# Performance work log

Measured on AMD Instinct MI355X. Metric: run time of the kernel, lower is better.

## Reference

```python
import jax, jax.numpy as jnp
import numpy as np

D_MODEL = 1024
N_HEADS = 16
HEAD_DIM = D_MODEL // N_HEADS


def setup_inputs() -> dict:
    key = jax.random.key(0)
    ks = jax.random.split(key, 5)
    x = jax.random.normal(ks[0], (2, 2048, D_MODEL), dtype=jnp.float32)
    s = 1.0 / np.sqrt(D_MODEL)
    W_qkv = jax.random.normal(ks[1], (D_MODEL, 3 * D_MODEL), dtype=jnp.float32) * s
    b_qkv = jnp.zeros((3 * D_MODEL,), dtype=jnp.float32)
    W_proj = jax.random.normal(ks[2], (D_MODEL, D_MODEL), dtype=jnp.float32) * s
    b_proj = jnp.zeros((D_MODEL,), dtype=jnp.float32)
    return {"x": x, "W_qkv": W_qkv, "b_qkv": b_qkv, "W_proj": W_proj, "b_proj": b_proj}


def reference(x, W_qkv, b_qkv, W_proj, b_proj):
    b, t, c = x.shape
    qkv = x @ W_qkv + b_qkv  # [b,t,3c]
    q, k, v = jnp.split(qkv, 3, axis=-1)
    # [b, h, t, d]
    q = q.reshape(b, t, N_HEADS, HEAD_DIM).transpose(0, 2, 1, 3)
    k = k.reshape(b, t, N_HEADS, HEAD_DIM).transpose(0, 2, 1, 3)
    v = v.reshape(b, t, N_HEADS, HEAD_DIM).transpose(0, 2, 1, 3)
    att = jnp.einsum('bhqd,bhkd->bhqk', q, k) / np.sqrt(HEAD_DIM)
    causal = jnp.tril(jnp.ones((t, t), dtype=bool))  # [t,t]
    att = jnp.where(causal[None, None], att, -jnp.inf)
    att = jax.nn.softmax(att, axis=-1)
    out = jnp.einsum('bhqk,bhkd->bhqd', att, v)  # [b,h,t,d]
    out = out.transpose(0, 2, 1, 3).reshape(b, t, c)
    return out @ W_proj + b_proj
```

## Files before the change

### kernel.cpp

```cpp
#include <hip/hip_runtime.h>
#include <hip/hip_bf16.h>

#define NB 2
#define NH 16
#define HD 64
#define DM 1024
#define TT 2048

typedef __attribute__((ext_vector_type(4))) float f32x4;
typedef __attribute__((ext_vector_type(8))) short bf16x8;

__device__ __forceinline__ unsigned short f2bf(float f) {
  union { float f; unsigned int i; } x; x.f = f;
  unsigned int r = x.i + 0x7fffu + ((x.i >> 16) & 1u);
  return (unsigned short)(r >> 16);
}

__device__ __forceinline__ unsigned int cvtpk(float lo, float hi) {
  unsigned int r;
  asm("v_cvt_pk_bf16_f32 %0, %1, %2" : "=v"(r) : "v"(lo), "v"(hi));
  return r;
}

__device__ __forceinline__ void async16(unsigned short* lds_base, const unsigned short* g) {
  __builtin_amdgcn_global_load_lds(
      (const __attribute__((address_space(1))) void*)g,
      (__attribute__((address_space(3))) void*)lds_base, 16, 0, 0);
}

__global__ __launch_bounds__(256)
void prep_kernel(const float* __restrict__ x, unsigned short* __restrict__ xbf,
                 const float* __restrict__ Wqkv, unsigned short* __restrict__ WqkvT,
                 const float* __restrict__ Wproj, unsigned short* __restrict__ WprojT)
{
  __shared__ unsigned short T[64][72];
  const int bid = blockIdx.x;
  const int t = threadIdx.x;

  if (bid < 2048) {
    const int i = bid * 256 + t;
    const f32x4 a = *(const f32x4*)(x + (size_t)i * 8);
    const f32x4 b = *(const f32x4*)(x + (size_t)i * 8 + 4);
    uint4 o;
    o.x = f2bf(a.x) | ((unsigned)f2bf(a.y) << 16);
    o.y = f2bf(a.z) | ((unsigned)f2bf(a.w) << 16);
    o.z = f2bf(b.x) | ((unsigned)f2bf(b.y) << 16);
    o.w = f2bf(b.z) | ((unsigned)f2bf(b.w) << 16);
    *(uint4*)(xbf + (size_t)i * 8) = o;
    return;
  }

  const float* W;
  unsigned short* WT;
  int n0, k0, N;
  if (bid < 2048 + 768) {
    const int li = bid - 2048;
    W = Wqkv; WT = WqkvT; N = 3 * DM;
    n0 = (li % 48) * 64; k0 = (li / 48) * 64;
  } else {
    const int li = bid - 2816;
    W = Wproj; WT = WprojT; N = DM;
    n0 = (li % 16) * 64; k0 = (li / 16) * 64;
  }
  const int r = t >> 2;
  const int c = (t & 3) * 16;
  const float* src = W + (size_t)(k0 + r) * N + n0 + c;
  #pragma unroll
  for (int s = 0; s < 4; ++s) {
    const f32x4 v = *(const f32x4*)(src + s * 4);
    T[c + s*4 + 0][r] = f2bf(v.x);
    T[c + s*4 + 1][r] = f2bf(v.y);
    T[c + s*4 + 2][r] = f2bf(v.z);
    T[c + s*4 + 3][r] = f2bf(v.w);
  }
  __syncthreads();
  unsigned short* dst = WT + (size_t)(n0 + r) * DM + k0 + c;
  *(uint4*)(dst)     = *(const uint4*)(&T[r][c]);
  *(uint4*)(dst + 8) = *(const uint4*)(&T[r][c + 8]);
}

template<int MODE>
__global__ __launch_bounds__(256)
void gemm_bf16(const unsigned short* __restrict__ A, const unsigned short* __restrict__ BT,
               const float* __restrict__ bias, void* __restrict__ Cout,
               int M, int N, int K)
{
  __shared__ unsigned short As[128 * 32];
  __shared__ unsigned short Bs[128 * 32];
  const int tid = threadIdx.x;
  const int lane = tid & 63;
  const int w = tid >> 6;
  const int wr = w >> 1, wc = w & 1;
  const int l15 = lane & 15, g = lane >> 4;

  const int gx = gridDim.x;
  const int li = blockIdx.y * gx + blockIdx.x;
  const int chunk = (gx * gridDim.y) >> 3;
  const int tile = (li & 7) * chunk + (li >> 3);
  const int m0 = (tile / gx) * 128;
  const int n0 = (tile % gx) * 128;

  f32x4 acc[4][4] = {};

  const int ar0 = tid >> 2,          as0 = (tid & 3) * 8;
  const int ar1 = (256 + tid) >> 2;
  const unsigned short* A0 = A + (size_t)(m0 + ar0) * K + as0;
  const unsigned short* A1 = A + (size_t)(m0 + ar1) * K + as0;
  const unsigned short* B0 = BT + (size_t)(n0 + ar0) * K + as0;
  const unsigned short* B1 = BT + (size_t)(n0 + ar1) * K + as0;
  unsigned short* AsW0 = &As[(0 * 256 + w * 64) * 8];
  unsigned short* AsW1 = &As[(1 * 256 + w * 64) * 8];
  unsigned short* BsW0 = &Bs[(0 * 256 + w * 64) * 8];
  unsigned short* BsW1 = &Bs[(1 * 256 + w * 64) * 8];

  for (int k0 = 0; k0 < K; k0 += 32) {
    async16(AsW0, A0 + k0);
    async16(AsW1, A1 + k0);
    async16(BsW0, B0 + k0);
    async16(BsW1, B1 + k0);
    __syncthreads();

    bf16x8 af[4], bfv[4];
    #pragma unroll
    for (int i = 0; i < 4; ++i)
      af[i] = *(const bf16x8*)(&As[(wr * 64 + i * 16 + l15) * 32 + g * 8]);
    #pragma unroll
    for (int j = 0; j < 4; ++j)
      bfv[j] = *(const bf16x8*)(&Bs[(wc * 64 + j * 16 + l15) * 32 + g * 8]);
    #pragma unroll
    for (int i = 0; i < 4; ++i)
      #pragma unroll
      for (int j = 0; j < 4; ++j)
        acc[i][j] = __builtin_amdgcn_mfma_f32_16x16x32_bf16(af[i], bfv[j], acc[i][j], 0, 0, 0);
    __syncthreads();
  }

  #pragma unroll
  for (int i = 0; i < 4; ++i) {
    #pragma unroll
    for (int j = 0; j < 4; ++j) {
      #pragma unroll
      for (int e = 0; e < 4; ++e) {
        const int row = m0 + wr * 64 + i * 16 + g * 4 + e;
        const int col = n0 + wc * 64 + j * 16 + l15;
        float val = acc[i][j][e] + bias[col];
        if (MODE == 0) {
          const int which = col >> 10;
          if (which == 0) val *= 0.125f;
          const int rem = col & 1023;
          const int hh = rem >> 6, dd = rem & 63;
          const int bb = row >> 11, tt = row & 2047;
          ((unsigned short*)Cout)[((((size_t)which * NB + bb) * NH + hh) * TT + tt) * HD + dd] = f2bf(val);
        } else {
          ((float*)Cout)[(size_t)row * N + col] = val;
        }
      }
    }
  }
}

__global__ __launch_bounds__(512)
void attn_kernel(const unsigned short* __restrict__ qkv, unsigned short* __restrict__ attn_out)
{
  __shared__ unsigned short Ksm[64 * 72];
  __shared__ unsigned short VTsm[64 * 70];
  __shared__ unsigned short Psm[8][16 * 72];

  const int tid = threadIdx.x;
  const int lane = tid & 63;
  const int wv = tid >> 6;
  const int l15 = lane & 15;
  const int g = lane >> 4;

  const int li = blockIdx.x;
  const int xcd = li & 7;
  const int r = li >> 3;
  const int halfid = r >> 5;
  const int j = r & 31;
  const int bh = ((j >> 3) << 3) | xcd;
  const int jj = j & 7;
  const int qt = halfid ? (7 - jj) : (8 + jj);
  const int q0 = qt * 128;

  const size_t base = (size_t)bh * TT * HD;
  const unsigned short* Qg = qkv + base;
  const unsigned short* Kg = qkv + (size_t)NB * NH * TT * HD + base;
  const unsigned short* Vg = qkv + (size_t)2 * NB * NH * TT * HD + base;

  const int qw = q0 + wv * 16;
  const bf16x8 qf0 = *(const bf16x8*)(Qg + (size_t)(qw + l15) * HD + g * 8);
  const bf16x8 qf1 = *(const bf16x8*)(Qg + (size_t)(qw + l15) * HD + 32 + g * 8);

  f32x4 o[4] = {};
  float lsum = 0.f;

  const bool kRole = (wv < 4);
  const int krow = (tid & 255) >> 2;
  const int kseg = (tid & 3) * 16;
  const int vt   = tid & 255;
  const int vr0  = (vt >> 4) * 4;
  const int vc0  = (vt & 15) * 4;

  const int nt = 2 * qt + 2;

  uint4 st0, st1;
  {
    if (kRole) {
      const unsigned short* kp = Kg + (size_t)krow * HD + kseg;
      st0 = *(const uint4*)(kp);
      st1 = *(const uint4*)(kp + 8);
    } else {
      const uint2 a = *(const uint2*)(Vg + (size_t)(vr0 + 0) * HD + vc0);
      const uint2 b = *(const uint2*)(Vg + (size_t)(vr0 + 1) * HD + vc0);
      const uint2 c = *(const uint2*)(Vg + (size_t)(vr0 + 2) * HD + vc0);
      const uint2 d = *(const uint2*)(Vg + (size_t)(vr0 + 3) * HD + vc0);
      st0.x = a.x; st0.y = a.y; st0.z = b.x; st0.w = b.y;
      st1.x = c.x; st1.y = c.y; st1.z = d.x; st1.w = d.y;
    }
  }

  for (int t = 0; t < nt; ++t) {
    const int t0 = t * 64;
    __syncthreads();
    if (kRole) {
      *(uint4*)(&Ksm[krow * 72 + kseg])     = st0;
      *(uint4*)(&Ksm[krow * 72 + kseg + 8]) = st1;
    } else {
      unsigned short r0[4] = {(unsigned short)(st0.x & 0xffffu), (unsigned short)(st0.x >> 16),
                              (unsigned short)(st0.y & 0xffffu), (unsigned short)(st0.y >> 16)};
      unsigned short r1[4] = {(unsigned short)(st0.z & 0xffffu), (unsigned short)(st0.z >> 16),
                              (unsigned short)(st0.w & 0xffffu), (unsigned short)(st0.w >> 16)};
      unsigned short r2[4] = {(unsigned short)(st1.x & 0xffffu), (unsigned short)(st1.x >> 16),
                              (unsigned short)(st1.y & 0xffffu), (unsigned short)(st1.y >> 16)};
      unsigned short r3[4] = {(unsigned short)(st1.z & 0xffffu), (unsigned short)(st1.z >> 16),
                              (unsigned short)(st1.w & 0xffffu), (unsigned short)(st1.w >> 16)};
      #pragma unroll
      for (int c2 = 0; c2 < 4; ++c2) {
        ushort4 col;
        col.x = r0[c2]; col.y = r1[c2]; col.z = r2[c2]; col.w = r3[c2];
        *(ushort4*)(&VTsm[(vc0 + c2) * 70 + vr0]) = col;
      }
    }
    __syncthreads();

    if (t + 1 < nt) {
      const int t1 = t0 + 64;
      if (kRole) {
        const unsigned short* kp = Kg + (size_t)(t1 + krow) * HD + kseg;
        st0 = *(const uint4*)(kp);
        st1 = *(const uint4*)(kp + 8);
      } else {
        const uint2 a = *(const uint2*)(Vg + (size_t)(t1 + vr0 + 0) * HD + vc0);
        const uint2 b = *(const uint2*)(Vg + (size_t)(t1 + vr0 + 1) * HD + vc0);
        const uint2 c = *(const uint2*)(Vg + (size_t)(t1 + vr0 + 2) * HD + vc0);
        const uint2 d = *(const uint2*)(Vg + (size_t)(t1 + vr0 + 3) * HD + vc0);
        st0.x = a.x; st0.y = a.y; st0.z = b.x; st0.w = b.y;
        st1.x = c.x; st1.y = c.y; st1.z = d.x; st1.w = d.y;
      }
    }

    if (t0 <= qw + 15) {
      f32x4 sT[4] = {};
      __builtin_amdgcn_s_setprio(1);
      #pragma unroll
      for (int b = 0; b < 4; ++b) {
        const bf16x8 kf0 = *(const bf16x8*)(&Ksm[(b * 16 + l15) * 72 + g * 8]);
        const bf16x8 kf1 = *(const bf16x8*)(&Ksm[(b * 16 + l15) * 72 + 32 + g * 8]);
        sT[b] = __builtin_amdgcn_mfma_f32_16x16x32_bf16(kf0, qf0, sT[b], 0, 0, 0);
        sT[b] = __builtin_amdgcn_mfma_f32_16x16x32_bf16(kf1, qf1, sT[b], 0, 0, 0);
      }
      __builtin_amdgcn_s_setprio(0);

      if (t0 + 63 > qw) {
        #pragma unroll
        for (int b = 0; b < 4; ++b)
          #pragma unroll
          for (int e = 0; e < 4; ++e)
            if (t0 + b * 16 + 4 * g + e > qw + l15) sT[b][e] = -INFINITY;
      }

      #pragma unroll
      for (int b = 0; b < 4; ++b) {
        const float p0 = __expf(sT[b][0]);
        const float p1 = __expf(sT[b][1]);
        const float p2 = __expf(sT[b][2]);
        const float p3 = __expf(sT[b][3]);
        lsum += (p0 + p1) + (p2 + p3);
        uint2 wd; wd.x = cvtpk(p0, p1); wd.y = cvtpk(p2, p3);
        *(uint2*)(&Psm[wv][l15 * 72 + b * 16 + 4 * g]) = wd;
      }

      __builtin_amdgcn_s_setprio(1);
      #pragma unroll
      for (int c = 0; c < 2; ++c) {
        const bf16x8 pf = *(const bf16x8*)(&Psm[wv][l15 * 72 + c * 32 + g * 8]);
        #pragma unroll
        for (int db = 0; db < 4; ++db) {
          const bf16x8 vf = *(const bf16x8*)(&VTsm[(db * 16 + l15) * 70 + c * 32 + g * 8]);
          o[db] = __builtin_amdgcn_mfma_f32_16x16x32_bf16(pf, vf, o[db], 0, 0, 0);
        }
      }
      __builtin_amdgcn_s_setprio(0);
    }
  }

  lsum += __shfl_xor(lsum, 16, 64);
  lsum += __shfl_xor(lsum, 32, 64);

  const int bb = bh >> 4;
  const int hh = bh & 15;
  #pragma unroll
  for (int e = 0; e < 4; ++e) {
    const float inv = 1.f / __shfl(lsum, 4 * g + e, 64);
    const int q = qw + 4 * g + e;
    #pragma unroll
    for (int db = 0; db < 4; ++db)
      attn_out[(size_t)(bb * TT + q) * DM + hh * HD + db * 16 + l15] = f2bf(o[db][e] * inv);
  }
}

extern "C" void kernel_launch(void* const* d_in, const int* in_sizes, int n_in,
                              void* d_out, int out_size, void* d_ws, size_t ws_size,
                              hipStream_t stream)
{
  const float* x     = (const float*)d_in[0];
  const float* Wqkv  = (const float*)d_in[1];
  const float* bqkv  = (const float*)d_in[2];
  const float* Wproj = (const float*)d_in[3];
  const float* bproj = (const float*)d_in[4];

  const size_t qkv_elems = (size_t)3 * NB * NH * TT * HD;
  unsigned short* qkv_ws  = (unsigned short*)d_ws;
  unsigned short* WqkvT   = qkv_ws + qkv_elems;
  unsigned short* WprojT  = WqkvT + (size_t)3 * DM * DM;
  unsigned short* xbf     = WprojT + (size_t)DM * DM;
  unsigned short* attn_ws = xbf;

  hipLaunchKernelGGL(prep_kernel, dim3(3072, 1, 1), dim3(256), 0, stream,
                     x, xbf, Wqkv, WqkvT, Wproj, WprojT);
  hipLaunchKernelGGL((gemm_bf16<0>), dim3(3 * DM / 128, NB * TT / 128, 1), dim3(256), 0, stream,
                     xbf, WqkvT, bqkv, (void*)qkv_ws, NB * TT, 3 * DM, DM);
  hipLaunchKernelGGL(attn_kernel, dim3(512, 1, 1), dim3(512), 0, stream,
                     qkv_ws, attn_ws);
  hipLaunchKernelGGL((gemm_bf16<1>), dim3(DM / 128, NB * TT / 128, 1), dim3(256), 0, stream,
                     attn_ws, WprojT, bproj, d_out, NB * TT, DM, DM);
}
```

Baseline: 124.4 us.

## Split attention KV range into two halves with a separate merge kernel

Each (batch-head, query tile) attention block is split into two blocks. One covers the first half of the causal KV tiles and the other covers the rest, doubling the grid to 1024 blocks. Each block writes its unnormalized bf16 partial output and its row sums. A new merge kernel adds the two partials and normalizes them before the projection GEMM. The aim is more parallelism and shorter per-block critical paths, at the cost of an extra launch, extra global traffic for partials, and extra bf16 rounding of the unnormalized partials.

```diff
diff --git a/kernel.cpp b/kernel.cpp
--- a/kernel.cpp
+++ b/kernel.cpp
@@ -20,6 +20,13 @@
   unsigned int r;
   asm("v_cvt_pk_bf16_f32 %0, %1, %2" : "=v"(r) : "v"(lo), "v"(hi));
   return r;
+}
+
+__device__ __forceinline__ float bfLO(unsigned int w) {
+  union { unsigned int u; float f; } x; x.u = w << 16; return x.f;
+}
+__device__ __forceinline__ float bfHI(unsigned int w) {
+  union { unsigned int u; float f; } x; x.u = w & 0xffff0000u; return x.f;
 }
 
 __device__ __forceinline__ void async16(unsigned short* lds_base, const unsigned short* g) {
@@ -160,7 +167,9 @@
 }
 
 __global__ __launch_bounds__(512)
-void attn_kernel(const unsigned short* __restrict__ qkv, unsigned short* __restrict__ attn_out)
+void attn_kernel(const unsigned short* __restrict__ qkv,
+                 unsigned short* __restrict__ partA, unsigned short* __restrict__ partB,
+                 float* __restrict__ lA, float* __restrict__ lB)
 {
   __shared__ unsigned short Ksm[64 * 72];
   __shared__ unsigned short VTsm[64 * 70];
@@ -175,12 +184,16 @@
   const int li = blockIdx.x;
   const int xcd = li & 7;
   const int r = li >> 3;
-  const int halfid = r >> 5;
+  const int qd = r >> 5;
   const int j = r & 31;
   const int bh = ((j >> 3) << 3) | xcd;
   const int jj = j & 7;
-  const int qt = halfid ? (7 - jj) : (8 + jj);
+  const int qt = (qd < 2) ? (8 + jj) : (7 - jj);
+  const int half = qd & 1;
   const int q0 = qt * 128;
+
+  unsigned short* part = half ? partB : partA;
+  float* lp = half ? lB : lA;
 
   const size_t base = (size_t)bh * TT * HD;
   const unsigned short* Qg = qkv + base;
@@ -201,25 +214,27 @@
   const int vr0  = (vt >> 4) * 4;
   const int vc0  = (vt & 15) * 4;
 
-  const int nt = 2 * qt + 2;
+  const int tstart = half ? (qt + 1) : 0;
+  const int tend   = half ? (2 * qt + 2) : (qt + 1);
 
   uint4 st0, st1;
   {
+    const int tb = tstart * 64;
     if (kRole) {
-      const unsigned short* kp = Kg + (size_t)krow * HD + kseg;
+      const unsigned short* kp = Kg + (size_t)(tb + krow) * HD + kseg;
       st0 = *(const uint4*)(kp);
       st1 = *(const uint4*)(kp + 8);
     } else {
-      const uint2 a = *(const uint2*)(Vg + (size_t)(vr0 + 0) * HD + vc0);
-      const uint2 b = *(const uint2*)(Vg + (size_t)(vr0 + 1) * HD + vc0);
-      const uint2 c = *(const uint2*)(Vg + (size_t)(vr0 + 2) * HD + vc0);
-      const uint2 d = *(const uint2*)(Vg + (size_t)(vr0 + 3) * HD + vc0);
+      const uint2 a = *(const uint2*)(Vg + (size_t)(tb + vr0 + 0) * HD + vc0);
+      const uint2 b = *(const uint2*)(Vg + (size_t)(tb + vr0 + 1) * HD + vc0);
+      const uint2 c = *(const uint2*)(Vg + (size_t)(tb + vr0 + 2) * HD + vc0);
+      const uint2 d = *(const uint2*)(Vg + (size_t)(tb + vr0 + 3) * HD + vc0);
       st0.x = a.x; st0.y = a.y; st0.z = b.x; st0.w = b.y;
       st1.x = c.x; st1.y = c.y; st1.z = d.x; st1.w = d.y;
     }
   }
 
-  for (int t = 0; t < nt; ++t) {
+  for (int t = tstart; t < tend; ++t) {
     const int t0 = t * 64;
     __syncthreads();
     if (kRole) {
@@ -243,7 +258,7 @@
     }
     __syncthreads();
 
-    if (t + 1 < nt) {
+    if (t + 1 < tend) {
       const int t1 = t0 + 64;
       if (kRole) {
         const unsigned short* kp = Kg + (size_t)(t1 + krow) * HD + kseg;
@@ -306,17 +321,41 @@
 
   lsum += __shfl_xor(lsum, 16, 64);
   lsum += __shfl_xor(lsum, 32, 64);
+  if (g == 0) lp[(size_t)bh * TT + qw + l15] = lsum;
 
   const int bb = bh >> 4;
   const int hh = bh & 15;
   #pragma unroll
   for (int e = 0; e < 4; ++e) {
-    const float inv = 1.f / __shfl(lsum, 4 * g + e, 64);
     const int q = qw + 4 * g + e;
     #pragma unroll
     for (int db = 0; db < 4; ++db)
-      attn_out[(size_t)(bb * TT + q) * DM + hh * HD + db * 16 + l15] = f2bf(o[db][e] * inv);
-  }
+      part[(size_t)(bb * TT + q) * DM + hh * HD + db * 16 + l15] = f2bf(o[db][e]);
+  }
+}
+
+__global__ __launch_bounds__(256)
+void merge_kernel(const unsigned short* __restrict__ A, const unsigned short* __restrict__ B,
+                  const float* __restrict__ lA, const float* __restrict__ lB,
+                  unsigned short* __restrict__ out)
+{
+  const int idx = blockIdx.x * 256 + threadIdx.x;
+  const size_t e8 = (size_t)idx * 8;
+  const int row = idx >> 7;
+  const int col = (idx & 127) * 8;
+  const int hh = col >> 6;
+  const int bb = row >> 11;
+  const int t = row & 2047;
+  const float inv = 1.f / (lA[(size_t)(bb * NH + hh) * TT + t] +
+                           lB[(size_t)(bb * NH + hh) * TT + t]);
+  const uint4 a = *(const uint4*)(A + e8);
+  const uint4 b = *(const uint4*)(B + e8);
+  uint4 o;
+  o.x = cvtpk((bfLO(a.x) + bfLO(b.x)) * inv, (bfHI(a.x) + bfHI(b.x)) * inv);
+  o.y = cvtpk((bfLO(a.y) + bfLO(b.y)) * inv, (bfHI(a.y) + bfHI(b.y)) * inv);
+  o.z = cvtpk((bfLO(a.z) + bfLO(b.z)) * inv, (bfHI(a.z) + bfHI(b.z)) * inv);
+  o.w = cvtpk((bfLO(a.w) + bfLO(b.w)) * inv, (bfHI(a.w) + bfHI(b.w)) * inv);
+  *(uint4*)(out + e8) = o;
 }
 
 extern "C" void kernel_launch(void* const* d_in, const int* in_sizes, int n_in,
@@ -329,19 +368,26 @@
   const float* Wproj = (const float*)d_in[3];
   const float* bproj = (const float*)d_in[4];
 
-  const size_t qkv_elems = (size_t)3 * NB * NH * TT * HD;
+  const size_t QE = (size_t)3 * NB * NH * TT * HD;
+  const size_t XE = (size_t)NB * TT * DM;
   unsigned short* qkv_ws  = (unsigned short*)d_ws;
-  unsigned short* WqkvT   = qkv_ws + qkv_elems;
+  unsigned short* WqkvT   = qkv_ws + QE;
   unsigned short* WprojT  = WqkvT + (size_t)3 * DM * DM;
   unsigned short* xbf     = WprojT + (size_t)DM * DM;
-  unsigned short* attn_ws = xbf;
+  unsigned short* partB   = xbf;
+  unsigned short* partA   = xbf + XE;
+  float* lA = (float*)(partA + XE);
+  float* lB = lA + (size_t)NB * NH * TT;
+  unsigned short* merged  = qkv_ws;
 
   hipLaunchKernelGGL(prep_kernel, dim3(3072, 1, 1), dim3(256), 0, stream,
                      x, xbf, Wqkv, WqkvT, Wproj, WprojT);
   hipLaunchKernelGGL((gemm_bf16<0>), dim3(3 * DM / 128, NB * TT / 128, 1), dim3(256), 0, stream,
                      xbf, WqkvT, bqkv, (void*)qkv_ws, NB * TT, 3 * DM, DM);
-  hipLaunchKernelGGL(attn_kernel, dim3(512, 1, 1), dim3(512), 0, stream,
-                     qkv_ws, attn_ws);
+  hipLaunchKernelGGL(attn_kernel, dim3(1024, 1, 1), dim3(512), 0, stream,
+                     qkv_ws, partA, partB, lA, lB);
+  hipLaunchKernelGGL(merge_kernel, dim3(2048, 1, 1), dim3(256), 0, stream,
+                     partA, partB, lA, lB, merged);
   hipLaunchKernelGGL((gemm_bf16<1>), dim3(DM / 128, NB * TT / 128, 1), dim3(256), 0, stream,
-                     attn_ws, WprojT, bproj, d_out, NB * TT, DM, DM);
-}
+                     merged, WprojT, bproj, d_out, NB * TT, DM, DM);
+}
```

Measured after the change: 133.2 us. 1.07x slower.
